# Optimization experiments

Measured on AMD Instinct MI355X. Metric: run time of the kernel, lower is better.

Reference implementation:

```python
import jax, jax.numpy as jnp
import numpy as np

N_NODES = 100000
N_EDGES = 1600000
D_FEAT = 64


def setup_inputs() -> dict:
    key = jax.random.key(0)
    k1, k2, k3 = jax.random.split(key, 3)
    features = jax.random.normal(k1, (N_NODES, D_FEAT), dtype=jnp.float32)
    row = jax.random.randint(k2, (N_EDGES,), 0, N_NODES, dtype=jnp.int64 if jax.config.jax_enable_x64 else jnp.int32)
    col = jax.random.randint(k3, (N_EDGES,), 0, N_NODES, dtype=jnp.int64 if jax.config.jax_enable_x64 else jnp.int32)
    return {"features": features, "row": row, "col": col}


def reference(features, row, col):
    # adj @ H  ==  segment-sum of H[col] grouped by row (COO SpMM)
    n = features.shape[0]
    gathered = features[col]                                  # [E, d] irregular gather
    summed = jax.ops.segment_sum(gathered, row, num_segments=n)  # [N, d]
    # deg = clip(adj.sum(1), 1, None) -> per-row nonzero count
    ones = jnp.ones((row.shape[0],), dtype=features.dtype)
    deg = jax.ops.segment_sum(ones, row, num_segments=n)
    deg = jnp.clip(deg, 1.0, None)
    agg = summed / deg[:, None]
    # combine: residual add
    return features + agg
```

## Files before the change

kernel.cpp:

```cpp
#include <hip/hip_runtime.h>

#define D_FEAT 64
#define CB 256
#define CBITS 8
#define NBC 448
#define E_BLK 8192
#define TMAX 256
#define SCAP 4608
#define PKN 5

__device__ inline unsigned short f2bf(float f) {
    unsigned u = __float_as_uint(f);
    u += 0x7FFFu + ((u >> 16) & 1u);
    return (unsigned short)(u >> 16);
}
__device__ inline float bf_lo(unsigned u) { return __uint_as_float(u << 16); }
__device__ inline float bf_hi(unsigned u) { return __uint_as_float(u & 0xFFFF0000u); }

__global__ __launch_bounds__(1024, 8)
void bin8_conv_kernel(const int* __restrict__ row, const int* __restrict__ col,
                      int* __restrict__ tilebuf,
                      int* __restrict__ csumG,
                      int n_edges, int ebt, int nb2,
                      const float* __restrict__ feat,
                      unsigned short* __restrict__ feat_bf, int n4) {
    int gb = blockIdx.x;
    int t = threadIdx.x;
    if (gb < ebt) {
        __shared__ int hist[NBC];
        __shared__ int ebuf[E_BLK];
        __shared__ int wpart[16];
        int w = t >> 6, lane = t & 63;
        for (int i = t; i < NBC; i += 1024) hist[i] = 0;
        __syncthreads();
        int e0 = gb * E_BLK;
        int ne = min(E_BLK, n_edges - e0);
        int rr[8], cc[8];
        #pragma unroll
        for (int k = 0; k < 8; ++k) {
            int i = t + k * 1024;
            if (i < ne) { rr[k] = row[e0 + i]; cc[k] = col[e0 + i]; }
            else rr[k] = -1;
        }
        #pragma unroll
        for (int k = 0; k < 8; ++k)
            if (rr[k] >= 0) atomicAdd(&hist[rr[k] >> CBITS], 1);
        __syncthreads();
        int idx = w * 64 + lane;
        int v = 0, incl = 0;
        if (w < 7) {
            v = hist[idx];
            incl = v;
            #pragma unroll
            for (int o = 1; o < 64; o <<= 1) {
                int up = __shfl_up(incl, o, 64);
                if (lane >= o) incl += up;
            }
            if (lane == 63) wpart[w] = incl;
        }
        __syncthreads();
        if (t == 0) {
            int run = 0;
            #pragma unroll
            for (int k = 0; k < 7; ++k) { int x = wpart[k]; wpart[k] = run; run += x; }
        }
        __syncthreads();
        if (w < 7) {
            int excl = incl - v + wpart[w];
            if (idx < nb2) {
                csumG[(size_t)gb * (nb2 + 1) + idx] = excl;
                hist[idx] = excl;
            }
        }
        if (t == 0) csumG[(size_t)gb * (nb2 + 1) + nb2] = ne;
        __syncthreads();
        #pragma unroll
        for (int k = 0; k < 8; ++k) {
            if (rr[k] >= 0) {
                int b = rr[k] >> CBITS;
                int pos = atomicAdd(&hist[b], 1);
                ebuf[pos] = ((rr[k] & (CB - 1)) << 17) | cc[k];
            }
        }
        __syncthreads();
        for (int i = t; i < ne; i += 1024)
            tilebuf[(size_t)gb * E_BLK + i] = ebuf[i];
    } else {
        int i = (gb - ebt) * 1024 + t;
        if (i < n4) {
            float4 f = reinterpret_cast<const float4*>(feat)[i];
            ushort4 u;
            u.x = f2bf(f.x); u.y = f2bf(f.y); u.z = f2bf(f.z); u.w = f2bf(f.w);
            reinterpret_cast<ushort4*>(feat_bf)[i] = u;
        }
    }
}

template<int BF>
__global__ __launch_bounds__(1024, 8)
void agg10_kernel(const float* __restrict__ feat,
                  const unsigned short* __restrict__ feat_bf,
                  const int* __restrict__ tilebuf,
                  const int* __restrict__ csumG,
                  float* __restrict__ out, int n_nodes, int ebt, int nb2) {
    __shared__ int tstart[TMAX], tlen[TMAX], psum[TMAX];
    __shared__ int scol[SCAP];
    __shared__ int cnt[CB], incl[CB], cur[CB], ddeg[CB];
    __shared__ int wpart[16];

    int cb = blockIdx.x;
    int t = threadIdx.x;
    int w = t >> 6, lane = t & 63;
    int q = lane >> 3, sub = lane & 7;
    int rA = w * 16 + q;
    int rB = rA + 8;

    for (int i = t; i < TMAX; i += 1024) {
        int s = 0, l = 0;
        if (i < ebt) {
            s = csumG[(size_t)i * (nb2 + 1) + cb];
            l = csumG[(size_t)i * (nb2 + 1) + cb + 1] - s;
        }
        tstart[i] = s; tlen[i] = l;
    }
    if (t < CB) ddeg[t] = 0;
    __syncthreads();
    {
        int idx = w * 64 + lane;
        int v = 0, ic = 0;
        if (w < 4) {
            v = tlen[idx];
            ic = v;
            #pragma unroll
            for (int o = 1; o < 64; o <<= 1) {
                int up = __shfl_up(ic, o, 64);
                if (lane >= o) ic += up;
            }
            if (lane == 63) wpart[w] = ic;
        }
        __syncthreads();
        if (t == 0) {
            int run = 0;
            #pragma unroll
            for (int k = 0; k < 4; ++k) { int x = wpart[k]; wpart[k] = run; run += x; }
        }
        __syncthreads();
        if (w < 4) psum[idx] = ic + wpart[w];
        __syncthreads();
    }
    int total = psum[ebt - 1];

    float acc[16];
    #pragma unroll
    for (int k = 0; k < 16; ++k) acc[k] = 0.f;

#define GATHER(cv, o0)                                                         \
    do {                                                                       \
        if (BF) {                                                              \
            uint4 d = *reinterpret_cast<const uint4*>(                         \
                feat_bf + (size_t)(cv)*D_FEAT + sub * 8);                      \
            acc[o0+0] += bf_lo(d.x); acc[o0+1] += bf_hi(d.x);                  \
            acc[o0+2] += bf_lo(d.y); acc[o0+3] += bf_hi(d.y);                  \
            acc[o0+4] += bf_lo(d.z); acc[o0+5] += bf_hi(d.z);                  \
            acc[o0+6] += bf_lo(d.w); acc[o0+7] += bf_hi(d.w);                  \
        } else {                                                               \
            float4 x0 = *reinterpret_cast<const float4*>(                      \
                feat + (size_t)(cv)*D_FEAT + sub * 8);                         \
            float4 x1 = *reinterpret_cast<const float4*>(                      \
                feat + (size_t)(cv)*D_FEAT + sub * 8 + 4);                     \
            acc[o0+0] += x0.x; acc[o0+1] += x0.y;                              \
            acc[o0+2] += x0.z; acc[o0+3] += x0.w;                              \
            acc[o0+4] += x1.x; acc[o0+5] += x1.y;                              \
            acc[o0+6] += x1.z; acc[o0+7] += x1.w;                              \
        }                                                                      \
    } while (0)

    for (int L = 0; L < total; L += SCAP) {
        int R = min(L + SCAP, total);
        if (t < CB) cnt[t] = 0;
        __syncthreads();
        int pkr[PKN];
        #pragma unroll
        for (int k = 0; k < PKN; ++k) {
            int j = L + t + k * 1024;
            pkr[k] = -1;
            if (j < R) {
                int lo = 0, hi = ebt - 1;
                while (lo < hi) { int mid = (lo + hi) >> 1;
                                  if (psum[mid] > j) hi = mid; else lo = mid + 1; }
                int local = j - (psum[lo] - tlen[lo]);
                pkr[k] = tilebuf[(size_t)lo * E_BLK + tstart[lo] + local];
            }
        }
        #pragma unroll
        for (int k = 0; k < PKN; ++k)
            if (pkr[k] >= 0) atomicAdd(&cnt[((unsigned)pkr[k]) >> 17], 1);
        __syncthreads();
        {
            int idx = w * 64 + lane;
            int v = 0, ic = 0;
            if (w < 4) {
                v = cnt[idx];
                ic = v;
                #pragma unroll
                for (int o = 1; o < 64; o <<= 1) {
                    int up = __shfl_up(ic, o, 64);
                    if (lane >= o) ic += up;
                }
                if (lane == 63) wpart[w] = ic;
            }
            __syncthreads();
            if (t == 0) {
                int run = 0;
                #pragma unroll
                for (int k = 0; k < 4; ++k) { int x = wpart[k]; wpart[k] = run; run += x; }
            }
            __syncthreads();
            if (w < 4) {
                int ival = ic + wpart[w];
                incl[idx] = ival;
                cur[idx] = ival - v;
                ddeg[idx] += v;
            }
            __syncthreads();
        }
        #pragma unroll
        for (int k = 0; k < PKN; ++k) {
            if (pkr[k] >= 0) {
                int key = ((unsigned)pkr[k]) >> 17;
                scol[atomicAdd(&cur[key], 1)] = pkr[k] & 0x1FFFF;
            }
        }
        __syncthreads();
        int cA = cnt[rA], sA = incl[rA] - cA;
        int cB2 = cnt[rB], sB = incl[rB] - cB2;
        int m = max(cA, cB2);
        for (int j = 0; j < m; j += 2) {
            int c00 = (j < cA)      ? scol[sA + j]     : -1;
            int c01 = (j + 1 < cA)  ? scol[sA + j + 1] : -1;
            int c10 = (j < cB2)     ? scol[sB + j]     : -1;
            int c11 = (j + 1 < cB2) ? scol[sB + j + 1] : -1;
            if (c00 >= 0) GATHER(c00, 0);
            if (c10 >= 0) GATHER(c10, 8);
            if (c01 >= 0) GATHER(c01, 0);
            if (c11 >= 0) GATHER(c11, 8);
        }
        __syncthreads();
    }
#undef GATHER

    {
        int r = cb * CB + rA;
        if (r < n_nodes) {
            float inv = 1.0f / fmaxf((float)ddeg[rA], 1.0f);
            size_t off = (size_t)r * D_FEAT + sub * 8;
            float4 f0 = *reinterpret_cast<const float4*>(feat + off);
            float4 f1 = *reinterpret_cast<const float4*>(feat + off + 4);
            float4 o0, o1;
            o0.x = f0.x + acc[0] * inv; o0.y = f0.y + acc[1] * inv;
            o0.z = f0.z + acc[2] * inv; o0.w = f0.w + acc[3] * inv;
            o1.x = f1.x + acc[4] * inv; o1.y = f1.y + acc[5] * inv;
            o1.z = f1.z + acc[6] * inv; o1.w = f1.w + acc[7] * inv;
            *reinterpret_cast<float4*>(out + off) = o0;
            *reinterpret_cast<float4*>(out + off + 4) = o1;
        }
        r = cb * CB + rB;
        if (r < n_nodes) {
            float inv = 1.0f / fmaxf((float)ddeg[rB], 1.0f);
            size_t off = (size_t)r * D_FEAT + sub * 8;
            float4 f0 = *reinterpret_cast<const float4*>(feat + off);
            float4 f1 = *reinterpret_cast<const float4*>(feat + off + 4);
            float4 o0, o1;
            o0.x = f0.x + acc[8]  * inv; o0.y = f0.y + acc[9]  * inv;
            o0.z = f0.z + acc[10] * inv; o0.w = f0.w + acc[11] * inv;
            o1.x = f1.x + acc[12] * inv; o1.y = f1.y + acc[13] * inv;
            o1.z = f1.z + acc[14] * inv; o1.w = f1.w + acc[15] * inv;
            *reinterpret_cast<float4*>(out + off) = o0;
            *reinterpret_cast<float4*>(out + off + 4) = o1;
        }
    }
}

extern "C" void kernel_launch(void* const* d_in, const int* in_sizes, int n_in,
                              void* d_out, int out_size, void* d_ws, size_t ws_size,
                              hipStream_t stream) {
    const float* feat = (const float*)d_in[0];
    const int* row = (const int*)d_in[1];
    const int* col = (const int*)d_in[2];
    float* out = (float*)d_out;

    const int n_nodes = in_sizes[0] / D_FEAT;
    const int n_edges = in_sizes[1];
    const int nb2 = (n_nodes + CB - 1) / CB;
    const int ebt = (n_edges + E_BLK - 1) / E_BLK;
    const int n4 = n_nodes * D_FEAT / 4;

    size_t tb_bytes  = (size_t)ebt * E_BLK * 4;
    size_t cs_bytes  = (size_t)ebt * (nb2 + 1) * 4;
    size_t bf_bytes  = (size_t)n_nodes * D_FEAT * 2;

    size_t lean_need = tb_bytes + cs_bytes + 256;
    size_t fat_need  = lean_need + ((bf_bytes + 63) & ~(size_t)63);
    bool fat = (ws_size >= fat_need);

    char* ws = (char*)d_ws;
    size_t p = 0;
    int* tilebuf = (int*)(ws + p); p += tb_bytes;
    int* csumG   = (int*)(ws + p); p += cs_bytes;
    p = (p + 63) & ~(size_t)63;
    unsigned short* feat_bf = nullptr;
    if (fat) { feat_bf = (unsigned short*)(ws + p); }

    {
        int conv_blocks = fat ? (n4 + 1023) / 1024 : 0;
        bin8_conv_kernel<<<ebt + conv_blocks, 1024, 0, stream>>>(
            row, col, tilebuf, csumG, n_edges, ebt, nb2,
            feat, feat_bf, fat ? n4 : 0);
    }
    if (fat) {
        agg10_kernel<1><<<nb2, 1024, 0, stream>>>(
            feat, feat_bf, tilebuf, csumG, out, n_nodes, ebt, nb2);
    } else {
        agg10_kernel<0><<<nb2, 1024, 0, stream>>>(
            feat, nullptr, tilebuf, csumG, out, n_nodes, ebt, nb2);
    }
}
```

Before: 127.5 us.

## Split each row bucket across two half-blocks and unroll edge gather by four

The aggregation kernel now launches two 512-thread blocks per 256-row bucket. Each block handles 128 rows and keeps only the edges whose destination row falls in its half. This doubles the number of blocks to improve load balance and occupancy across CUs, and shrinks the shared-memory staging buffer. The gather loop is also unrolled to four edges per row per iteration to put more loads in flight. The cost is that both halves scan the bucket's full edge list, doing the binary search and tilebuf reads twice, and each block may now need more staging passes.

```diff
diff --git a/kernel.cpp b/kernel.cpp
--- a/kernel.cpp
+++ b/kernel.cpp
@@ -3,10 +3,11 @@
 #define D_FEAT 64
 #define CB 256
 #define CBITS 8
+#define HB 128
 #define NBC 448
 #define E_BLK 8192
 #define TMAX 256
-#define SCAP 4608
+#define SCAP 2560
 #define PKN 5
 
 __device__ inline unsigned short f2bf(float f) {
@@ -97,25 +98,28 @@
 }
 
 template<int BF>
-__global__ __launch_bounds__(1024, 8)
-void agg10_kernel(const float* __restrict__ feat,
+__global__ __launch_bounds__(512, 8)
+void agg11_kernel(const float* __restrict__ feat,
                   const unsigned short* __restrict__ feat_bf,
                   const int* __restrict__ tilebuf,
                   const int* __restrict__ csumG,
                   float* __restrict__ out, int n_nodes, int ebt, int nb2) {
     __shared__ int tstart[TMAX], tlen[TMAX], psum[TMAX];
     __shared__ int scol[SCAP];
-    __shared__ int cnt[CB], incl[CB], cur[CB], ddeg[CB];
-    __shared__ int wpart[16];
-
-    int cb = blockIdx.x;
+    __shared__ int cnt[HB], incl[HB], cur[HB], ddeg[HB];
+    __shared__ int wpart[8];
+
+    int blk = blockIdx.x;
+    int cb = blk >> 1;
+    int half = blk & 1;
     int t = threadIdx.x;
     int w = t >> 6, lane = t & 63;
-    int q = lane >> 3, sub = lane & 7;
-    int rA = w * 16 + q;
-    int rB = rA + 8;
-
-    for (int i = t; i < TMAX; i += 1024) {
+    int g = w * 8 + (lane >> 3);
+    int sub = lane & 7;
+    int rA = g;
+    int rB = g + 64;
+
+    for (int i = t; i < TMAX; i += 512) {
         int s = 0, l = 0;
         if (i < ebt) {
             s = csumG[(size_t)i * (nb2 + 1) + cb];
@@ -123,7 +127,7 @@
         }
         tstart[i] = s; tlen[i] = l;
     }
-    if (t < CB) ddeg[t] = 0;
+    if (t < HB) ddeg[t] = 0;
     __syncthreads();
     {
         int idx = w * 64 + lane;
@@ -177,29 +181,30 @@
 
     for (int L = 0; L < total; L += SCAP) {
         int R = min(L + SCAP, total);
-        if (t < CB) cnt[t] = 0;
+        if (t < HB) cnt[t] = 0;
         __syncthreads();
         int pkr[PKN];
         #pragma unroll
         for (int k = 0; k < PKN; ++k) {
-            int j = L + t + k * 1024;
+            int j = L + t + k * 512;
             pkr[k] = -1;
             if (j < R) {
                 int lo = 0, hi = ebt - 1;
                 while (lo < hi) { int mid = (lo + hi) >> 1;
                                   if (psum[mid] > j) hi = mid; else lo = mid + 1; }
                 int local = j - (psum[lo] - tlen[lo]);
-                pkr[k] = tilebuf[(size_t)lo * E_BLK + tstart[lo] + local];
+                int pk = tilebuf[(size_t)lo * E_BLK + tstart[lo] + local];
+                if ((int)(((unsigned)pk) >> 17 >> 7) == half) pkr[k] = pk;
             }
         }
         #pragma unroll
         for (int k = 0; k < PKN; ++k)
-            if (pkr[k] >= 0) atomicAdd(&cnt[((unsigned)pkr[k]) >> 17], 1);
+            if (pkr[k] >= 0) atomicAdd(&cnt[(((unsigned)pkr[k]) >> 17) & (HB - 1)], 1);
         __syncthreads();
         {
             int idx = w * 64 + lane;
             int v = 0, ic = 0;
-            if (w < 4) {
+            if (w < 2) {
                 v = cnt[idx];
                 ic = v;
                 #pragma unroll
@@ -210,13 +215,9 @@
                 if (lane == 63) wpart[w] = ic;
             }
             __syncthreads();
-            if (t == 0) {
-                int run = 0;
-                #pragma unroll
-                for (int k = 0; k < 4; ++k) { int x = wpart[k]; wpart[k] = run; run += x; }
-            }
+            if (t == 0) { int x = wpart[0]; wpart[0] = 0; wpart[1] = x; }
             __syncthreads();
-            if (w < 4) {
+            if (w < 2) {
                 int ival = ic + wpart[w];
                 incl[idx] = ival;
                 cur[idx] = ival - v;
@@ -227,7 +228,7 @@
         #pragma unroll
         for (int k = 0; k < PKN; ++k) {
             if (pkr[k] >= 0) {
-                int key = ((unsigned)pkr[k]) >> 17;
+                int key = (((unsigned)pkr[k]) >> 17) & (HB - 1);
                 scol[atomicAdd(&cur[key], 1)] = pkr[k] & 0x1FFFF;
             }
         }
@@ -235,22 +236,31 @@
         int cA = cnt[rA], sA = incl[rA] - cA;
         int cB2 = cnt[rB], sB = incl[rB] - cB2;
         int m = max(cA, cB2);
-        for (int j = 0; j < m; j += 2) {
+        for (int j = 0; j < m; j += 4) {
             int c00 = (j < cA)      ? scol[sA + j]     : -1;
             int c01 = (j + 1 < cA)  ? scol[sA + j + 1] : -1;
+            int c02 = (j + 2 < cA)  ? scol[sA + j + 2] : -1;
+            int c03 = (j + 3 < cA)  ? scol[sA + j + 3] : -1;
             int c10 = (j < cB2)     ? scol[sB + j]     : -1;
             int c11 = (j + 1 < cB2) ? scol[sB + j + 1] : -1;
+            int c12 = (j + 2 < cB2) ? scol[sB + j + 2] : -1;
+            int c13 = (j + 3 < cB2) ? scol[sB + j + 3] : -1;
             if (c00 >= 0) GATHER(c00, 0);
             if (c10 >= 0) GATHER(c10, 8);
             if (c01 >= 0) GATHER(c01, 0);
             if (c11 >= 0) GATHER(c11, 8);
+            if (c02 >= 0) GATHER(c02, 0);
+            if (c12 >= 0) GATHER(c12, 8);
+            if (c03 >= 0) GATHER(c03, 0);
+            if (c13 >= 0) GATHER(c13, 8);
         }
         __syncthreads();
     }
 #undef GATHER
 
+    int r0 = cb * CB + half * HB;
     {
-        int r = cb * CB + rA;
+        int r = r0 + rA;
         if (r < n_nodes) {
             float inv = 1.0f / fmaxf((float)ddeg[rA], 1.0f);
             size_t off = (size_t)r * D_FEAT + sub * 8;
@@ -264,7 +274,7 @@
             *reinterpret_cast<float4*>(out + off) = o0;
             *reinterpret_cast<float4*>(out + off + 4) = o1;
         }
-        r = cb * CB + rB;
+        r = r0 + rB;
         if (r < n_nodes) {
             float inv = 1.0f / fmaxf((float)ddeg[rB], 1.0f);
             size_t off = (size_t)r * D_FEAT + sub * 8;
@@ -318,10 +328,10 @@
             feat, feat_bf, fat ? n4 : 0);
     }
     if (fat) {
-        agg10_kernel<1><<<nb2, 1024, 0, stream>>>(
+        agg11_kernel<1><<<nb2 * 2, 512, 0, stream>>>(
             feat, feat_bf, tilebuf, csumG, out, n_nodes, ebt, nb2);
     } else {
-        agg10_kernel<0><<<nb2, 1024, 0, stream>>>(
+        agg11_kernel<0><<<nb2 * 2, 512, 0, stream>>>(
             feat, nullptr, tilebuf, csumG, out, n_nodes, ebt, nb2);
     }
 }
```

Measured after the change: 167.7 us. 1.32x slower.
